# Kernel tuning notes

Measured on AMD Instinct MI355X. Metric: run time of the kernel, lower is better.

Reference implementation:

```python
import jax, jax.numpy as jnp
import numpy as np

N_CLASS = 29   # len('SE?abcdefghijklmnopqrstuvwxyz')
N_HIDDEN = 128


def _rnn(x, h0, Wih, Whh, bih, bhh):
    """PyTorch nn.RNN (tanh, 1 layer, batch_first) semantics.
    x: [B,T,I], h0: [B,H]. Returns (outputs [B,T,H], h_T [B,H]).
    h_t = tanh(x_t @ Wih^T + bih + h_{t-1} @ Whh^T + bhh)
    """
    # Precompute input projection for all timesteps (batched GEMM).
    xp = jnp.einsum('bti,hi->bth', x, Wih) + (bih + bhh)  # [B,T,H]

    def step(h, xt):  # xt: [B,H]
        h_new = jnp.tanh(xt + h @ Whh.T)
        return h_new, h_new

    hT, hs = jax.lax.scan(step, h0, jnp.swapaxes(xp, 0, 1))  # scan over T
    return jnp.swapaxes(hs, 0, 1), hT


def setup_inputs() -> dict:
    key = jax.random.key(0)
    ks = jax.random.split(key, 12)
    B, T = 2048, 256
    s = 1.0 / np.sqrt(N_HIDDEN)  # PyTorch RNN/Linear init scale
    inp = {
        'encoder_input': jax.random.normal(ks[0], (B, T, N_CLASS), jnp.float32),
        'encoder_hidden': jnp.zeros((1, B, N_HIDDEN), jnp.float32),
        'decoder_input': jax.random.normal(ks[1], (B, T, N_CLASS), jnp.float32),
        'enc_Wih': jax.random.uniform(ks[2], (N_HIDDEN, N_CLASS), jnp.float32, -s, s),
        'enc_Whh': jax.random.uniform(ks[3], (N_HIDDEN, N_HIDDEN), jnp.float32, -s, s),
        'enc_bih': jax.random.uniform(ks[4], (N_HIDDEN,), jnp.float32, -s, s),
        'enc_bhh': jax.random.uniform(ks[5], (N_HIDDEN,), jnp.float32, -s, s),
        'dec_Wih': jax.random.uniform(ks[6], (N_HIDDEN, N_CLASS), jnp.float32, -s, s),
        'dec_Whh': jax.random.uniform(ks[7], (N_HIDDEN, N_HIDDEN), jnp.float32, -s, s),
        'dec_bih': jax.random.uniform(ks[8], (N_HIDDEN,), jnp.float32, -s, s),
        'dec_bhh': jax.random.uniform(ks[9], (N_HIDDEN,), jnp.float32, -s, s),
        'fc_W': jax.random.uniform(ks[10], (N_CLASS, N_HIDDEN), jnp.float32, -s, s),
        'fc_b': jax.random.uniform(ks[11], (N_CLASS,), jnp.float32, -s, s),
    }
    return inp


def reference(encoder_input, encoder_hidden, decoder_input,
              enc_Wih, enc_Whh, enc_bih, enc_bhh,
              dec_Wih, dec_Whh, dec_bih, dec_bhh,
              fc_W, fc_b):
    h0 = encoder_hidden[0]                                   # [B,H]
    _, h_t = _rnn(encoder_input, h0, enc_Wih, enc_Whh, enc_bih, enc_bhh)
    dec_out, _ = _rnn(decoder_input, h_t, dec_Wih, dec_Whh, dec_bih, dec_bhh)  # [B,T,H]
    return jnp.einsum('bth,ch->btc', dec_out, fc_W) + fc_b   # [B,T,n_class]
```

## Files before the change

kernel.cpp:

```cpp
#include <hip/hip_runtime.h>
#include <math.h>

#define TT 256
#define NI 29
#define HH 128
#define NC 29
#define ROWS 16
#define PSTR 136
#define BBATCH 2048L
#define WS_NEED (BBATCH * TT * HH * 2)

typedef _Float16 f16x8 __attribute__((ext_vector_type(8)));
typedef _Float16 f16x4 __attribute__((ext_vector_type(4)));
typedef float f32x4 __attribute__((ext_vector_type(4)));

__device__ __forceinline__ float fast_tanh(float x) {
    float ax = fabsf(x);
    float e = __builtin_amdgcn_exp2f(ax * -2.885390081777927f);
    float r = (1.0f - e) * __builtin_amdgcn_rcpf(1.0f + e);
    return copysignf(r, x);
}

__device__ __forceinline__ void load_x(const float* p, int g, float4& a, float4& b) {
    a = *(const float4*)p;
    if (g < 3) {
        b = *(const float4*)(p + 4);
    } else {
        b.x = p[4];
        b.y = 0.f; b.z = 0.f; b.w = 0.f;
    }
}

__device__ __forceinline__ f16x8 cvt8(const float4& a, const float4& b) {
    f16x8 r;
    r[0] = (_Float16)a.x; r[1] = (_Float16)a.y;
    r[2] = (_Float16)a.z; r[3] = (_Float16)a.w;
    r[4] = (_Float16)b.x; r[5] = (_Float16)b.y;
    r[6] = (_Float16)b.z; r[7] = (_Float16)b.w;
    return r;
}

#define MFMA16(A, B, C) __builtin_amdgcn_mfma_f32_16x16x32_f16((A), (B), (C), 0, 0, 0)

__launch_bounds__(256)
__global__ void xp_kernel(const float* __restrict__ x,
                          const float* __restrict__ Wih,
                          _Float16* __restrict__ xp)
{
    const int tid  = threadIdx.x;
    const int lane = tid & 63;
    const int wv   = tid >> 6;
    const int m    = lane & 15;
    const int g    = lane >> 4;
    const long bt0 = ((long)blockIdx.x * 4 + wv) * 16;

    f16x8 A[8];
#pragma unroll
    for (int jt = 0; jt < 8; ++jt) {
        float4 v0, v1;
        load_x(Wih + (16 * jt + m) * NI + 8 * g, g, v0, v1);
        A[jt] = cvt8(v0, v1);
    }
    float4 u0, u1;
    load_x(x + (bt0 + m) * NI + 8 * g, g, u0, u1);
    f16x8 Bx = cvt8(u0, u1);

    f32x4 z = {0.f, 0.f, 0.f, 0.f};
    f32x4 acc[8];
#pragma unroll
    for (int jt = 0; jt < 8; ++jt)
        acc[jt] = MFMA16(A[jt], Bx, z);

#pragma unroll
    for (int jt = 0; jt < 8; ++jt) {
        f16x4 o;
        o[0] = (_Float16)acc[jt][0];
        o[1] = (_Float16)acc[jt][1];
        o[2] = (_Float16)acc[jt][2];
        o[3] = (_Float16)acc[jt][3];
        *(f16x4*)(xp + (bt0 + m) * HH + 16 * jt + 4 * g) = o;
    }
}

#define STEP(CUR, XQ, X0, X1, TV)                                             \
  {                                                                           \
    f16x4 nx = {(_Float16)0, (_Float16)0, (_Float16)0, (_Float16)0};          \
    if (USE_XP) {                                                             \
      if ((TV) + 2 < TT) nx = *(const f16x4*)(xpro + ((TV) + 2) * HH);        \
    }                                                                         \
    f16x8 bx;                                                                 \
    if (!USE_XP) {                                                            \
      bx = cvt8(X0, X1);                                                      \
      if ((TV) + 2 < TT) load_x(xrow + ((TV) + 2) * NI, g, X0, X1);           \
    }                                                                         \
    f16x8 Bh[4];                                                              \
    _Pragma("unroll") for (int s = 0; s < 4; ++s)                             \
      Bh[s] = *(const f16x8*)&planes[CUR][m][32 * s + 8 * g];                 \
    f32x4 c0 = {0.f,0.f,0.f,0.f}, c1 = {0.f,0.f,0.f,0.f};                     \
    if (!USE_XP) c0 = MFMA16(Aw4, bx, c0);                                    \
    c0 = MFMA16(Aw[0], Bh[0], c0);                                            \
    c1 = MFMA16(Aw[1], Bh[1], c1);                                            \
    c0 = MFMA16(Aw[2], Bh[2], c0);                                            \
    c1 = MFMA16(Aw[3], Bh[3], c1);                                            \
    if (IS_DEC && fcw >= 0 && (TV) > 0) {                                     \
      f32x4 f0 = {0.f,0.f,0.f,0.f}, f1 = {0.f,0.f,0.f,0.f};                   \
      f0 = MFMA16(Afc[0], Bh[0], f0);                                         \
      f1 = MFMA16(Afc[1], Bh[1], f1);                                         \
      f0 = MFMA16(Afc[2], Bh[2], f0);                                         \
      f1 = MFMA16(Afc[3], Bh[3], f1);                                         \
      _Pragma("unroll") for (int q = 0; q < 4; ++q) {                         \
        int c = 16 * fcw + 4 * g + q;                                         \
        if (c < NC)                                                           \
          out[((long)(b0 + m) * TT + ((TV) - 1)) * NC + c] =                  \
              f0[q] + f1[q] + fcbv[q];                                        \
      }                                                                       \
    }                                                                         \
    f16x4 hhi;                                                                \
    _Pragma("unroll") for (int q = 0; q < 4; ++q) {                           \
      float aq = c0[q] + c1[q] + bias[q];                                     \
      if (USE_XP) aq += (float)XQ[q];                                         \
      hhi[q] = (_Float16)fast_tanh(aq);                                       \
    }                                                                         \
    *(f16x4*)&planes[CUR ^ 1][m][16 * w + 4 * g] = hhi;                       \
    asm volatile("s_waitcnt lgkmcnt(0)" ::: "memory");                        \
    __builtin_amdgcn_s_barrier();                                             \
    __builtin_amdgcn_sched_barrier(0);                                        \
    XQ = nx;                                                                  \
  }

template <int IS_DEC, int USE_XP>
__launch_bounds__(512, 1)
__global__ void rnn_mfma(const float* __restrict__ xin,
                         const _Float16* __restrict__ xp,
                         const float* __restrict__ h0p, long h0s,
                         const float* __restrict__ Wih,
                         const float* __restrict__ Whh,
                         const float* __restrict__ bih,
                         const float* __restrict__ bhh,
                         const float* __restrict__ fcW,
                         const float* __restrict__ fcb,
                         float* __restrict__ out)
{
    __shared__ __align__(16) _Float16 planes[2][ROWS][PSTR];

    const int tid  = threadIdx.x;
    const int lane = tid & 63;
    const int w    = tid >> 6;
    const int m    = lane & 15;
    const int g    = lane >> 4;
    const int b0   = blockIdx.x * ROWS;

    const int jr = 16 * w + m;
    f16x8 Aw[4];
#pragma unroll
    for (int s = 0; s < 4; ++s) {
        const float* src = Whh + jr * HH + 32 * s + 8 * g;
        float4 v0 = *(const float4*)src;
        float4 v1 = *(const float4*)(src + 4);
        Aw[s] = cvt8(v0, v1);
    }
    f16x8 Aw4;
    if (!USE_XP) {
        float4 v0, v1;
        load_x(Wih + jr * NI + 8 * g, g, v0, v1);
        Aw4 = cvt8(v0, v1);
    }
    float bias[4];
#pragma unroll
    for (int q = 0; q < 4; ++q)
        bias[q] = bih[16 * w + 4 * g + q] + bhh[16 * w + 4 * g + q];

    const int fcw = w - 6;
    f16x8 Afc[4];
    float fcbv[4] = {0.f, 0.f, 0.f, 0.f};
    if (IS_DEC && fcw >= 0) {
        int c = 16 * fcw + m;
#pragma unroll
        for (int s = 0; s < 4; ++s) {
            f16x8 a;
#pragma unroll
            for (int e = 0; e < 8; ++e) {
                int k = 32 * s + 8 * g + e;
                a[e] = (c < NC) ? (_Float16)fcW[c * HH + k] : (_Float16)0.f;
            }
            Afc[s] = a;
        }
#pragma unroll
        for (int q = 0; q < 4; ++q) {
            int c2 = 16 * fcw + 4 * g + q;
            fcbv[q] = (c2 < NC) ? fcb[c2] : 0.f;
        }
    }

    {
        int b  = tid >> 5;
        int i0 = (tid & 31) * 4;
        const float* hr = h0p + (long)(b0 + b) * h0s + i0;
        float4 v = *(const float4*)hr;
        f16x4 hq;
        hq[0] = (_Float16)v.x; hq[1] = (_Float16)v.y;
        hq[2] = (_Float16)v.z; hq[3] = (_Float16)v.w;
        *(f16x4*)&planes[0][b][i0] = hq;
    }

    const _Float16* xpro = xp + ((long)(b0 + m) * TT) * HH + 16 * w + 4 * g;
    const float*    xrow = xin + ((long)(b0 + m) * TT) * NI + 8 * g;
    f16x4 xqa = {(_Float16)0, (_Float16)0, (_Float16)0, (_Float16)0};
    f16x4 xqb = xqa;
    float4 xa0, xa1, xb0, xb1;
    if (USE_XP) {
        xqa = *(const f16x4*)(xpro);
        xqb = *(const f16x4*)(xpro + HH);
    } else {
        load_x(xrow + 0 * NI, g, xa0, xa1);
        load_x(xrow + 1 * NI, g, xb0, xb1);
    }
    __syncthreads();

    for (int t = 0; t < TT; t += 2) {
        STEP(0, xqa, xa0, xa1, t);
        STEP(1, xqb, xb0, xb1, t + 1);
    }

    if (IS_DEC) {
        if (fcw >= 0) {
            f16x8 Bh[4];
#pragma unroll
            for (int s = 0; s < 4; ++s)
                Bh[s] = *(const f16x8*)&planes[0][m][32 * s + 8 * g];
            f32x4 f0 = {0.f,0.f,0.f,0.f}, f1 = {0.f,0.f,0.f,0.f};
            f0 = MFMA16(Afc[0], Bh[0], f0);
            f1 = MFMA16(Afc[1], Bh[1], f1);
            f0 = MFMA16(Afc[2], Bh[2], f0);
            f1 = MFMA16(Afc[3], Bh[3], f1);
#pragma unroll
            for (int q = 0; q < 4; ++q) {
                int c = 16 * fcw + 4 * g + q;
                if (c < NC)
                    out[((long)(b0 + m) * TT + (TT - 1)) * NC + c] =
                        f0[q] + f1[q] + fcbv[q];
            }
        }
    } else {
        int b  = tid >> 5;
        int i0 = (tid & 31) * 4;
        float4 v;
        v.x = (float)planes[0][b][i0 + 0];
        v.y = (float)planes[0][b][i0 + 1];
        v.z = (float)planes[0][b][i0 + 2];
        v.w = (float)planes[0][b][i0 + 3];
        *(float4*)(out + (long)(b0 + b) * TT * NC + i0) = v;
    }
}

extern "C" void kernel_launch(void* const* d_in, const int* in_sizes, int n_in,
                              void* d_out, int out_size, void* d_ws, size_t ws_size,
                              hipStream_t stream) {
    const float* enc_in  = (const float*)d_in[0];
    const float* enc_h0  = (const float*)d_in[1];
    const float* dec_in  = (const float*)d_in[2];
    const float* enc_Wih = (const float*)d_in[3];
    const float* enc_Whh = (const float*)d_in[4];
    const float* enc_bih = (const float*)d_in[5];
    const float* enc_bhh = (const float*)d_in[6];
    const float* dec_Wih = (const float*)d_in[7];
    const float* dec_Whh = (const float*)d_in[8];
    const float* dec_bih = (const float*)d_in[9];
    const float* dec_bhh = (const float*)d_in[10];
    const float* fc_W    = (const float*)d_in[11];
    const float* fc_b    = (const float*)d_in[12];
    float* out = (float*)d_out;

    dim3 grid(BBATCH / ROWS), block(512);
    const bool fast = (ws_size >= (size_t)WS_NEED);

    if (fast) {
        _Float16* xp = (_Float16*)d_ws;
        dim3 xgrid((unsigned)(BBATCH * TT / 64)), xblock(256);
        xp_kernel<<<xgrid, xblock, 0, stream>>>(enc_in, enc_Wih, xp);
        rnn_mfma<0, 1><<<grid, block, 0, stream>>>(enc_in, xp, enc_h0, (long)HH,
                                                   enc_Wih, enc_Whh, enc_bih, enc_bhh,
                                                   nullptr, nullptr, out);
        xp_kernel<<<xgrid, xblock, 0, stream>>>(dec_in, dec_Wih, xp);
        rnn_mfma<1, 1><<<grid, block, 0, stream>>>(dec_in, xp, out, (long)TT * NC,
                                                   dec_Wih, dec_Whh, dec_bih, dec_bhh,
                                                   fc_W, fc_b, out);
    } else {
        rnn_mfma<0, 0><<<grid, block, 0, stream>>>(enc_in, nullptr, enc_h0, (long)HH,
                                                   enc_Wih, enc_Whh, enc_bih, enc_bhh,
                                                   nullptr, nullptr, out);
        rnn_mfma<1, 0><<<grid, block, 0, stream>>>(dec_in, nullptr, out, (long)TT * NC,
                                                   dec_Wih, dec_Whh, dec_bih, dec_bhh,
                                                   fc_W, fc_b, out);
    }
}
```

Baseline: 506.6 us.

## Halve RNN block to 4 waves, each computing two hidden tiles per step

Shrinks the recurrent block from 8 to 4 wavefronts, so each wave owns 32 hidden units and issues two interleaved MFMA chains per step. The FC projection moves to waves 0-1 and the loop unrolls by 4 with a 4-step input prefetch. tanh is rewritten without abs/copysign to save a few ALU ops, at some risk of overflow when the exp2 argument is large. The intent is cheaper per-step barriers and more independent MFMAs per wave, traded for more register pressure and fewer waves to hide latency.

Result: faster. 472.2 us (-6.8%).

```diff
diff --git a/kernel.cpp b/kernel.cpp
--- a/kernel.cpp
+++ b/kernel.cpp
@@ -15,10 +15,8 @@
 typedef float f32x4 __attribute__((ext_vector_type(4)));
 
 __device__ __forceinline__ float fast_tanh(float x) {
-    float ax = fabsf(x);
-    float e = __builtin_amdgcn_exp2f(ax * -2.885390081777927f);
-    float r = (1.0f - e) * __builtin_amdgcn_rcpf(1.0f + e);
-    return copysignf(r, x);
+    float e = __builtin_amdgcn_exp2f(x * 2.885390081777927f);
+    return 1.0f - 2.0f * __builtin_amdgcn_rcpf(e + 1.0f);
 }
 
 __device__ __forceinline__ void load_x(const float* p, int g, float4& a, float4& b) {
@@ -82,54 +80,58 @@
     }
 }
 
-#define STEP(CUR, XQ, X0, X1, TV)                                             \
+#define STEP(CUR, XQA, XQB, XFA, XFB, TV)                                     \
   {                                                                           \
-    f16x4 nx = {(_Float16)0, (_Float16)0, (_Float16)0, (_Float16)0};          \
-    if (USE_XP) {                                                             \
-      if ((TV) + 2 < TT) nx = *(const f16x4*)(xpro + ((TV) + 2) * HH);        \
+    f16x8 Bh0 = *(const f16x8*)&planes[CUR][m][ 0 + 8 * g];                   \
+    f16x8 Bh1 = *(const f16x8*)&planes[CUR][m][32 + 8 * g];                   \
+    f16x8 Bh2 = *(const f16x8*)&planes[CUR][m][64 + 8 * g];                   \
+    f16x8 Bh3 = *(const f16x8*)&planes[CUR][m][96 + 8 * g];                   \
+    f32x4 c00 = {0.f,0.f,0.f,0.f}, c01 = {0.f,0.f,0.f,0.f};                   \
+    f32x4 c10 = {0.f,0.f,0.f,0.f}, c11 = {0.f,0.f,0.f,0.f};                   \
+    if (!USE_XP) {                                                            \
+      f16x8 bx = cvt8(XFA, XFB);                                              \
+      c00 = MFMA16(AwX0, bx, c00);                                            \
+      c10 = MFMA16(AwX1, bx, c10);                                            \
+      if ((TV) + 4 < TT) load_x(xrow + ((TV) + 4) * NI, g, XFA, XFB);         \
     }                                                                         \
-    f16x8 bx;                                                                 \
-    if (!USE_XP) {                                                            \
-      bx = cvt8(X0, X1);                                                      \
-      if ((TV) + 2 < TT) load_x(xrow + ((TV) + 2) * NI, g, X0, X1);           \
-    }                                                                         \
-    f16x8 Bh[4];                                                              \
-    _Pragma("unroll") for (int s = 0; s < 4; ++s)                             \
-      Bh[s] = *(const f16x8*)&planes[CUR][m][32 * s + 8 * g];                 \
-    f32x4 c0 = {0.f,0.f,0.f,0.f}, c1 = {0.f,0.f,0.f,0.f};                     \
-    if (!USE_XP) c0 = MFMA16(Aw4, bx, c0);                                    \
-    c0 = MFMA16(Aw[0], Bh[0], c0);                                            \
-    c1 = MFMA16(Aw[1], Bh[1], c1);                                            \
-    c0 = MFMA16(Aw[2], Bh[2], c0);                                            \
-    c1 = MFMA16(Aw[3], Bh[3], c1);                                            \
-    if (IS_DEC && fcw >= 0 && (TV) > 0) {                                     \
+    c00 = MFMA16(Aw0[0], Bh0, c00);  c10 = MFMA16(Aw1[0], Bh0, c10);          \
+    c01 = MFMA16(Aw0[1], Bh1, c01);  c11 = MFMA16(Aw1[1], Bh1, c11);          \
+    c00 = MFMA16(Aw0[2], Bh2, c00);  c10 = MFMA16(Aw1[2], Bh2, c10);          \
+    c01 = MFMA16(Aw0[3], Bh3, c01);  c11 = MFMA16(Aw1[3], Bh3, c11);          \
+    if (IS_DEC && w < 2 && (TV) > 0) {                                        \
       f32x4 f0 = {0.f,0.f,0.f,0.f}, f1 = {0.f,0.f,0.f,0.f};                   \
-      f0 = MFMA16(Afc[0], Bh[0], f0);                                         \
-      f1 = MFMA16(Afc[1], Bh[1], f1);                                         \
-      f0 = MFMA16(Afc[2], Bh[2], f0);                                         \
-      f1 = MFMA16(Afc[3], Bh[3], f1);                                         \
+      f0 = MFMA16(Afc[0], Bh0, f0);                                           \
+      f1 = MFMA16(Afc[1], Bh1, f1);                                           \
+      f0 = MFMA16(Afc[2], Bh2, f0);                                           \
+      f1 = MFMA16(Afc[3], Bh3, f1);                                           \
       _Pragma("unroll") for (int q = 0; q < 4; ++q) {                         \
-        int c = 16 * fcw + 4 * g + q;                                         \
+        int c = 16 * w + 4 * g + q;                                           \
         if (c < NC)                                                           \
           out[((long)(b0 + m) * TT + ((TV) - 1)) * NC + c] =                  \
               f0[q] + f1[q] + fcbv[q];                                        \
       }                                                                       \
     }                                                                         \
-    f16x4 hhi;                                                                \
+    f16x4 hn0, hn1;                                                           \
     _Pragma("unroll") for (int q = 0; q < 4; ++q) {                           \
-      float aq = c0[q] + c1[q] + bias[q];                                     \
-      if (USE_XP) aq += (float)XQ[q];                                         \
-      hhi[q] = (_Float16)fast_tanh(aq);                                       \
+      float a0 = c00[q] + c01[q] + bias0[q];                                  \
+      float a1 = c10[q] + c11[q] + bias1[q];                                  \
+      if (USE_XP) { a0 += (float)XQA[q]; a1 += (float)XQB[q]; }               \
+      hn0[q] = (_Float16)fast_tanh(a0);                                       \
+      hn1[q] = (_Float16)fast_tanh(a1);                                       \
     }                                                                         \
-    *(f16x4*)&planes[CUR ^ 1][m][16 * w + 4 * g] = hhi;                       \
+    if (USE_XP && (TV) + 4 < TT) {                                            \
+      XQA = *(const f16x4*)(xpro + ((TV) + 4) * HH);                          \
+      XQB = *(const f16x4*)(xpro + ((TV) + 4) * HH + 16);                     \
+    }                                                                         \
+    *(f16x4*)&planes[CUR ^ 1][m][32 * w + 4 * g]      = hn0;                  \
+    *(f16x4*)&planes[CUR ^ 1][m][32 * w + 16 + 4 * g] = hn1;                  \
     asm volatile("s_waitcnt lgkmcnt(0)" ::: "memory");                        \
     __builtin_amdgcn_s_barrier();                                             \
     __builtin_amdgcn_sched_barrier(0);                                        \
-    XQ = nx;                                                                  \
   }
 
 template <int IS_DEC, int USE_XP>
-__launch_bounds__(512, 1)
+__launch_bounds__(256, 1)
 __global__ void rnn_mfma(const float* __restrict__ xin,
                          const _Float16* __restrict__ xp,
                          const float* __restrict__ h0p, long h0s,
@@ -150,31 +152,38 @@
     const int g    = lane >> 4;
     const int b0   = blockIdx.x * ROWS;
 
-    const int jr = 16 * w + m;
-    f16x8 Aw[4];
+    f16x8 Aw0[4], Aw1[4];
 #pragma unroll
     for (int s = 0; s < 4; ++s) {
-        const float* src = Whh + jr * HH + 32 * s + 8 * g;
-        float4 v0 = *(const float4*)src;
-        float4 v1 = *(const float4*)(src + 4);
-        Aw[s] = cvt8(v0, v1);
-    }
-    f16x8 Aw4;
+        const float* s0 = Whh + (32 * w + m) * HH + 32 * s + 8 * g;
+        const float* s1 = Whh + (32 * w + 16 + m) * HH + 32 * s + 8 * g;
+        float4 v0 = *(const float4*)s0;
+        float4 v1 = *(const float4*)(s0 + 4);
+        Aw0[s] = cvt8(v0, v1);
+        float4 u0 = *(const float4*)s1;
+        float4 u1 = *(const float4*)(s1 + 4);
+        Aw1[s] = cvt8(u0, u1);
+    }
+    f16x8 AwX0, AwX1;
     if (!USE_XP) {
         float4 v0, v1;
-        load_x(Wih + jr * NI + 8 * g, g, v0, v1);
-        Aw4 = cvt8(v0, v1);
-    }
-    float bias[4];
-#pragma unroll
-    for (int q = 0; q < 4; ++q)
-        bias[q] = bih[16 * w + 4 * g + q] + bhh[16 * w + 4 * g + q];
-
-    const int fcw = w - 6;
+        load_x(Wih + (32 * w + m) * NI + 8 * g, g, v0, v1);
+        AwX0 = cvt8(v0, v1);
+        load_x(Wih + (32 * w + 16 + m) * NI + 8 * g, g, v0, v1);
+        AwX1 = cvt8(v0, v1);
+    }
+    float bias0[4], bias1[4];
+#pragma unroll
+    for (int q = 0; q < 4; ++q) {
+        int j0 = 32 * w + 4 * g + q;
+        bias0[q] = bih[j0] + bhh[j0];
+        bias1[q] = bih[j0 + 16] + bhh[j0 + 16];
+    }
+
     f16x8 Afc[4];
     float fcbv[4] = {0.f, 0.f, 0.f, 0.f};
-    if (IS_DEC && fcw >= 0) {
-        int c = 16 * fcw + m;
+    if (IS_DEC && w < 2) {
+        int c = 16 * w + m;
 #pragma unroll
         for (int s = 0; s < 4; ++s) {
             f16x8 a;
@@ -187,69 +196,75 @@
         }
 #pragma unroll
         for (int q = 0; q < 4; ++q) {
-            int c2 = 16 * fcw + 4 * g + q;
+            int c2 = 16 * w + 4 * g + q;
             fcbv[q] = (c2 < NC) ? fcb[c2] : 0.f;
         }
     }
 
     {
-        int b  = tid >> 5;
-        int i0 = (tid & 31) * 4;
+        int b  = tid >> 4;
+        int i0 = (tid & 15) * 8;
         const float* hr = h0p + (long)(b0 + b) * h0s + i0;
-        float4 v = *(const float4*)hr;
-        f16x4 hq;
-        hq[0] = (_Float16)v.x; hq[1] = (_Float16)v.y;
-        hq[2] = (_Float16)v.z; hq[3] = (_Float16)v.w;
-        *(f16x4*)&planes[0][b][i0] = hq;
-    }
-
-    const _Float16* xpro = xp + ((long)(b0 + m) * TT) * HH + 16 * w + 4 * g;
+        float4 v0 = *(const float4*)hr;
+        float4 v1 = *(const float4*)(hr + 4);
+        *(f16x8*)&planes[0][b][i0] = cvt8(v0, v1);
+    }
+
+    const _Float16* xpro = xp + ((long)(b0 + m) * TT) * HH + 32 * w + 4 * g;
     const float*    xrow = xin + ((long)(b0 + m) * TT) * NI + 8 * g;
-    f16x4 xqa = {(_Float16)0, (_Float16)0, (_Float16)0, (_Float16)0};
-    f16x4 xqb = xqa;
-    float4 xa0, xa1, xb0, xb1;
+    f16x4 xqa0, xqb0, xqa1, xqb1, xqa2, xqb2, xqa3, xqb3;
+    float4 xf0a, xf0b, xf1a, xf1b, xf2a, xf2b, xf3a, xf3b;
     if (USE_XP) {
-        xqa = *(const f16x4*)(xpro);
-        xqb = *(const f16x4*)(xpro + HH);
+        xqa0 = *(const f16x4*)(xpro + 0 * HH); xqb0 = *(const f16x4*)(xpro + 0 * HH + 16);
+        xqa1 = *(const f16x4*)(xpro + 1 * HH); xqb1 = *(const f16x4*)(xpro + 1 * HH + 16);
+        xqa2 = *(const f16x4*)(xpro + 2 * HH); xqb2 = *(const f16x4*)(xpro + 2 * HH + 16);
+        xqa3 = *(const f16x4*)(xpro + 3 * HH); xqb3 = *(const f16x4*)(xpro + 3 * HH + 16);
     } else {
-        load_x(xrow + 0 * NI, g, xa0, xa1);
-        load_x(xrow + 1 * NI, g, xb0, xb1);
+        load_x(xrow + 0 * NI, g, xf0a, xf0b);
+        load_x(xrow + 1 * NI, g, xf1a, xf1b);
+        load_x(xrow + 2 * NI, g, xf2a, xf2b);
+        load_x(xrow + 3 * NI, g, xf3a, xf3b);
     }
     __syncthreads();
 
-    for (int t = 0; t < TT; t += 2) {
-        STEP(0, xqa, xa0, xa1, t);
-        STEP(1, xqb, xb0, xb1, t + 1);
+    for (int t = 0; t < TT; t += 4) {
+        STEP(0, xqa0, xqb0, xf0a, xf0b, t);
+        STEP(1, xqa1, xqb1, xf1a, xf1b, t + 1);
+        STEP(0, xqa2, xqb2, xf2a, xf2b, t + 2);
+        STEP(1, xqa3, xqb3, xf3a, xf3b, t + 3);
     }
 
     if (IS_DEC) {
-        if (fcw >= 0) {
-            f16x8 Bh[4];
-#pragma unroll
-            for (int s = 0; s < 4; ++s)
-                Bh[s] = *(const f16x8*)&planes[0][m][32 * s + 8 * g];
+        if (w < 2) {
+            f16x8 Bh0 = *(const f16x8*)&planes[0][m][ 0 + 8 * g];
+            f16x8 Bh1 = *(const f16x8*)&planes[0][m][32 + 8 * g];
+            f16x8 Bh2 = *(const f16x8*)&planes[0][m][64 + 8 * g];
+            f16x8 Bh3 = *(const f16x8*)&planes[0][m][96 + 8 * g];
             f32x4 f0 = {0.f,0.f,0.f,0.f}, f1 = {0.f,0.f,0.f,0.f};
-            f0 = MFMA16(Afc[0], Bh[0], f0);
-            f1 = MFMA16(Afc[1], Bh[1], f1);
-            f0 = MFMA16(Afc[2], Bh[2], f0);
-            f1 = MFMA16(Afc[3], Bh[3], f1);
+            f0 = MFMA16(Afc[0], Bh0, f0);
+            f1 = MFMA16(Afc[1], Bh1, f1);
+            f0 = MFMA16(Afc[2], Bh2, f0);
+            f1 = MFMA16(Afc[3], Bh3, f1);
 #pragma unroll
             for (int q = 0; q < 4; ++q) {
-                int c = 16 * fcw + 4 * g + q;
+                int c = 16 * w + 4 * g + q;
                 if (c < NC)
                     out[((long)(b0 + m) * TT + (TT - 1)) * NC + c] =
                         f0[q] + f1[q] + fcbv[q];
             }
         }
     } else {
-        int b  = tid >> 5;
-        int i0 = (tid & 31) * 4;
-        float4 v;
-        v.x = (float)planes[0][b][i0 + 0];
-        v.y = (float)planes[0][b][i0 + 1];
-        v.z = (float)planes[0][b][i0 + 2];
-        v.w = (float)planes[0][b][i0 + 3];
-        *(float4*)(out + (long)(b0 + b) * TT * NC + i0) = v;
+        int b  = tid >> 4;
+        int i0 = (tid & 15) * 8;
+        f16x8 hv = *(const f16x8*)&planes[0][b][i0];
+        float4 v0, v1;
+        v0.x = (float)hv[0]; v0.y = (float)hv[1];
+        v0.z = (float)hv[2]; v0.w = (float)hv[3];
+        v1.x = (float)hv[4]; v1.y = (float)hv[5];
+        v1.z = (float)hv[6]; v1.w = (float)hv[7];
+        float* dst = out + (long)(b0 + b) * TT * NC + i0;
+        *(float4*)dst = v0;
+        *(float4*)(dst + 4) = v1;
     }
 }
 
@@ -271,7 +286,7 @@
     const float* fc_b    = (const float*)d_in[12];
     float* out = (float*)d_out;
 
-    dim3 grid(BBATCH / ROWS), block(512);
+    dim3 grid(BBATCH / ROWS), block(256);
     const bool fast = (ws_size >= (size_t)WS_NEED);
 
     if (fast) {
```
